# Kernel optimization log

Hardware: AMD Instinct MI355X
Metric: run time of the kernel (lower is better)

Reference implementation:

```python
import jax, jax.numpy as jnp
import numpy as np
import math

B, T, C, H = 8, 1024, 1024, 16
D = C // H  # head dim = 64
EPS = 1e-5


def layernorm(x, g, b):
    mu = jnp.mean(x, axis=-1, keepdims=True)
    var = jnp.var(x, axis=-1, keepdims=True)
    return (x - mu) * jax.lax.rsqrt(var + EPS) * g + b


def setup_inputs() -> dict:
    key = jax.random.key(0)
    ks = jax.random.split(key, 8)
    s = lambda fan_in: 1.0 / math.sqrt(fan_in)
    return {
        "x": jax.random.normal(ks[0], (B, T, C), jnp.float32),
        "Wqkv": jax.random.normal(ks[1], (C, 3 * C), jnp.float32) * s(C),
        "bqkv": jnp.zeros((3 * C,), jnp.float32),
        "Wproj": jax.random.normal(ks[2], (C, C), jnp.float32) * s(C),
        "bproj": jnp.zeros((C,), jnp.float32),
        "ln1_g": jnp.ones((C,), jnp.float32),
        "ln1_b": jnp.zeros((C,), jnp.float32),
        "ln2_g": jnp.ones((C,), jnp.float32),
        "ln2_b": jnp.zeros((C,), jnp.float32),
        "W1": jax.random.normal(ks[3], (C, 4 * C), jnp.float32) * s(C),
        "b1": jnp.zeros((4 * C,), jnp.float32),
        "W2": jax.random.normal(ks[4], (4 * C, C), jnp.float32) * s(4 * C),
        "b2": jnp.zeros((C,), jnp.float32),
    }


def reference(x, Wqkv, bqkv, Wproj, bproj, ln1_g, ln1_b, ln2_g, ln2_b, W1, b1, W2, b2):
    # --- self-attention on ln1(x) ---
    h = layernorm(x, ln1_g, ln1_b)
    qkv = h @ Wqkv + bqkv                          # [B,T,3C]
    q, k, v = jnp.split(qkv, 3, axis=-1)
    # [B,T,C] -> [B,H,T,D]
    q = q.reshape(B, T, H, D).transpose(0, 2, 1, 3)
    k = k.reshape(B, T, H, D).transpose(0, 2, 1, 3)
    v = v.reshape(B, T, H, D).transpose(0, 2, 1, 3)
    # NOTE: original uses 1/sqrt(3*n_embd//n_head), not 1/sqrt(head_dim)
    scale = 1.0 / math.sqrt(3 * C // H)
    attn = jnp.einsum("bhqd,bhkd->bhqk", q, k) * scale  # [B,H,T,T]
    causal = jnp.tril(jnp.ones((T, T), bool))
    attn = jnp.where(causal, attn, -jnp.inf)
    attn = jax.nn.softmax(attn, axis=-1)
    y = jnp.einsum("bhqk,bhkd->bhqd", attn, v)          # [B,H,T,D]
    y = y.transpose(0, 2, 1, 3).reshape(B, T, C)
    x = x + (y @ Wproj + bproj)
    # --- MLP on ln2(x) ---
    h2 = layernorm(x, ln2_g, ln2_b)
    x = x + (jax.nn.relu(h2 @ W1 + b1) @ W2 + b2)
    return x
```

## Files before the change

kernel.cpp:

```cpp
#include <hip/hip_runtime.h>

typedef __bf16 bf16;
typedef __bf16 bf16x8 __attribute__((ext_vector_type(8)));
typedef float f32x4 __attribute__((ext_vector_type(4)));

#define MFMA16(a, b, c) __builtin_amdgcn_mfma_f32_16x16x32_bf16(a, b, c, 0, 0, 0)

static constexpr int Bn = 8;
static constexpr int Tn = 1024;
static constexpr int Cn = 1024;
static constexpr int Hn = 16;

typedef const __attribute__((address_space(1))) unsigned int* gp_t;
typedef __attribute__((address_space(3))) unsigned int* lp_t;
__device__ __forceinline__ void gload_lds16(const bf16* g, bf16* l) {
    __builtin_amdgcn_global_load_lds((gp_t)(const void*)g, (lp_t)(void*)l, 16, 0, 0);
}

__global__ __launch_bounds__(256) void tcast(const float* __restrict__ in,
                                             bf16* __restrict__ out,
                                             int K, int N) {
    __shared__ float tile[32][33];
    const int n0 = blockIdx.x * 32, k0 = blockIdx.y * 32;
    const int tx = threadIdx.x & 31, ty = threadIdx.x >> 5;
#pragma unroll
    for (int i = 0; i < 4; i++)
        tile[ty + 8 * i][tx] = in[(size_t)(k0 + ty + 8 * i) * N + n0 + tx];
    __syncthreads();
#pragma unroll
    for (int i = 0; i < 4; i++)
        out[(size_t)(n0 + ty + 8 * i) * K + k0 + tx] = (bf16)tile[tx][ty + 8 * i];
}

__global__ __launch_bounds__(256) void ln_bf16(const float* __restrict__ x,
                                               const float* __restrict__ g,
                                               const float* __restrict__ be,
                                               bf16* __restrict__ out) {
    const int row = blockIdx.x, t = threadIdx.x;
    const float* xr = x + (size_t)row * Cn;
    float v[4], s = 0.f, s2 = 0.f;
#pragma unroll
    for (int i = 0; i < 4; i++) {
        v[i] = xr[t + i * 256];
        s += v[i];
        s2 += v[i] * v[i];
    }
#pragma unroll
    for (int off = 32; off > 0; off >>= 1) {
        s += __shfl_down(s, off);
        s2 += __shfl_down(s2, off);
    }
    __shared__ float red[8];
    const int wave = t >> 6, lane = t & 63;
    if (lane == 0) {
        red[wave] = s;
        red[4 + wave] = s2;
    }
    __syncthreads();
    s = red[0] + red[1] + red[2] + red[3];
    s2 = red[4] + red[5] + red[6] + red[7];
    const float mu = s * (1.f / Cn);
    const float rstd = rsqrtf(s2 * (1.f / Cn) - mu * mu + 1e-5f);
    bf16* orow = out + (size_t)row * Cn;
#pragma unroll
    for (int i = 0; i < 4; i++) {
        int c = t + i * 256;
        orow[c] = (bf16)((v[i] - mu) * rstd * g[c] + be[c]);
    }
}

__global__ __launch_bounds__(256) void vtrans(const bf16* __restrict__ qkv,
                                              bf16* __restrict__ Vt) {
    __shared__ bf16 tile[64 * 72];
    const int tid = threadIdx.x;
    const int bh = blockIdx.x, b = bh >> 4, h = bh & 15;
    const int t0 = blockIdx.y * 64;
    const int r = tid >> 3, c = (tid & 7) * 8;
#pragma unroll
    for (int i = 0; i < 2; i++) {
        const int rr = r + i * 32;
        *(bf16x8*)(tile + rr * 72 + c) =
            *(const bf16x8*)(qkv + ((size_t)(b * Tn + t0 + rr)) * 3072 + 2 * Cn + h * 64 + c);
    }
    __syncthreads();
#pragma unroll
    for (int i = 0; i < 2; i++) {
        const int d = r + i * 32;
        bf16x8 v;
#pragma unroll
        for (int j = 0; j < 8; j++) v[j] = tile[(c + j) * 72 + d];
        *(bf16x8*)(Vt + ((size_t)bh * 64 + d) * Tn + t0 + c) = v;
    }
}

template <bool RELU, bool RESID, bool OUTBF16>
__global__ __launch_bounds__(256) void gemm_bt(const bf16* __restrict__ A,
                                               const bf16* __restrict__ Bt,
                                               const float* __restrict__ bias,
                                               const float* __restrict__ resid,
                                               void* __restrict__ outp,
                                               int M, int N, int K) {
    __shared__ __align__(16) bf16 As[128 * 32];
    __shared__ __align__(16) bf16 Bs[128 * 32];
    const int t = threadIdx.x;
    const int lane = t & 63, wave = t >> 6;
    const int lane15 = lane & 15, quad = lane >> 4;
    const int m0 = blockIdx.x * 128, n0 = blockIdx.y * 128;
    const int mb = (wave >> 1) * 64, nb = (wave & 1) * 64;

    const f32x4 zero4 = {0.f, 0.f, 0.f, 0.f};
    f32x4 acc[4][4];
#pragma unroll
    for (int i = 0; i < 4; i++)
#pragma unroll
        for (int j = 0; j < 4; j++) acc[i][j] = zero4;

    const int r16 = lane >> 2, c8 = (lane & 3) * 8;
    const bf16* gA0 = A + (size_t)(m0 + wave * 16 + r16) * K + c8;
    const bf16* gA1 = gA0 + (size_t)64 * K;
    const bf16* gB0 = Bt + (size_t)(n0 + wave * 16 + r16) * K + c8;
    const bf16* gB1 = gB0 + (size_t)64 * K;
    bf16* lA0 = As + wave * 512;
    bf16* lA1 = As + 2048 + wave * 512;
    bf16* lB0 = Bs + wave * 512;
    bf16* lB1 = Bs + 2048 + wave * 512;

    for (int kt = 0; kt < K; kt += 32) {
        gload_lds16(gA0 + kt, lA0);
        gload_lds16(gA1 + kt, lA1);
        gload_lds16(gB0 + kt, lB0);
        gload_lds16(gB1 + kt, lB1);
        __syncthreads();
        bf16x8 fa[4], fb[4];
#pragma unroll
        for (int mi = 0; mi < 4; mi++)
            fa[mi] = *(const bf16x8*)(As + (mb + mi * 16 + lane15) * 32 + quad * 8);
#pragma unroll
        for (int ni = 0; ni < 4; ni++)
            fb[ni] = *(const bf16x8*)(Bs + (nb + ni * 16 + lane15) * 32 + quad * 8);
#pragma unroll
        for (int mi = 0; mi < 4; mi++)
#pragma unroll
            for (int ni = 0; ni < 4; ni++)
                acc[mi][ni] = MFMA16(fa[mi], fb[ni], acc[mi][ni]);
        __syncthreads();
    }

    float bsv[4];
#pragma unroll
    for (int ni = 0; ni < 4; ni++) bsv[ni] = bias[n0 + nb + ni * 16 + lane15];
#pragma unroll
    for (int mi = 0; mi < 4; mi++) {
#pragma unroll
        for (int reg = 0; reg < 4; reg++) {
            const int row = m0 + mb + mi * 16 + quad * 4 + reg;
#pragma unroll
            for (int ni = 0; ni < 4; ni++) {
                const int col = n0 + nb + ni * 16 + lane15;
                float v = acc[mi][ni][reg] + bsv[ni];
                if (RELU) v = v > 0.f ? v : 0.f;
                if (RESID) v += resid[(size_t)row * N + col];
                if (OUTBF16)
                    ((bf16*)outp)[(size_t)row * N + col] = (bf16)v;
                else
                    ((float*)outp)[(size_t)row * N + col] = v;
            }
        }
    }
}

__global__ __launch_bounds__(256) void attn(const bf16* __restrict__ qkv,
                                            const bf16* __restrict__ Vt,
                                            bf16* __restrict__ y) {
    __shared__ __align__(16) bf16 Ks[64 * 72];
    __shared__ __align__(16) bf16 Vs[80 * 72];
    __shared__ __align__(16) bf16 Ps[4][32 * 72];
    const int tid = threadIdx.x, lane = tid & 63, wave = tid >> 6;
    const int lane15 = lane & 15, quad = lane >> 4;
    const int b = blockIdx.x >> 4, h = blockIdx.x & 15;
    const int q0 = blockIdx.y * 128;
    const int qr0 = q0 + wave * 32;
    const float c1 = 0.10412043f;

    for (int i = tid; i < 16 * 72; i += 256)
        Vs[64 * 72 + i] = (bf16)((i < 72) ? 1.0f : 0.0f);

    bf16x8 fq[2][2];
#pragma unroll
    for (int mi = 0; mi < 2; mi++) {
        const size_t qb = ((size_t)(b * Tn + qr0 + mi * 16 + lane15)) * 3072 + h * 64;
#pragma unroll
        for (int kk = 0; kk < 2; kk++)
            fq[mi][kk] = *(const bf16x8*)(qkv + qb + kk * 32 + quad * 8);
    }

    const f32x4 zero4 = {0.f, 0.f, 0.f, 0.f};
    f32x4 o[2][4], lacc[2];
#pragma unroll
    for (int mi = 0; mi < 2; mi++) {
        lacc[mi] = zero4;
#pragma unroll
        for (int ni = 0; ni < 4; ni++) o[mi][ni] = zero4;
    }

    const int sr = tid >> 3, sc = (tid & 7) * 8;
    const int nkb = q0 / 64 + 2;
    for (int kb = 0; kb < nkb; kb++) {
        const int k0 = kb * 64;
#pragma unroll
        for (int i = 0; i < 2; i++) {
            const int r = sr + i * 32;
            *(bf16x8*)(Ks + r * 72 + sc) =
                *(const bf16x8*)(qkv + ((size_t)(b * Tn + k0 + r)) * 3072 + Cn + h * 64 + sc);
            *(bf16x8*)(Vs + r * 72 + sc) =
                *(const bf16x8*)(Vt + ((size_t)blockIdx.x * 64 + r) * Tn + k0 + sc);
        }
        __syncthreads();

        if (k0 <= qr0 + 31) {
            bf16x8 fk[4][2];
#pragma unroll
            for (int ni = 0; ni < 4; ni++)
#pragma unroll
                for (int kk = 0; kk < 2; kk++)
                    fk[ni][kk] = *(const bf16x8*)(Ks + (ni * 16 + lane15) * 72 + kk * 32 + quad * 8);
            f32x4 s[2][4];
#pragma unroll
            for (int mi = 0; mi < 2; mi++)
#pragma unroll
                for (int ni = 0; ni < 4; ni++) {
                    f32x4 a = zero4;
                    a = MFMA16(fq[mi][0], fk[ni][0], a);
                    a = MFMA16(fq[mi][1], fk[ni][1], a);
                    s[mi][ni] = a;
                }
            const bool domask = (k0 + 63 > qr0);
            if (domask) {
#pragma unroll
                for (int mi = 0; mi < 2; mi++)
#pragma unroll
                    for (int ni = 0; ni < 4; ni++)
#pragma unroll
                        for (int r = 0; r < 4; r++) {
                            const int key = k0 + ni * 16 + lane15;
                            const int row = qr0 + mi * 16 + quad * 4 + r;
                            float L = (key > row) ? -1e30f : s[mi][ni][r] * c1;
                            Ps[wave][(mi * 16 + quad * 4 + r) * 72 + ni * 16 + lane15] =
                                (bf16)__builtin_amdgcn_exp2f(L);
                        }
            } else {
#pragma unroll
                for (int mi = 0; mi < 2; mi++)
#pragma unroll
                    for (int ni = 0; ni < 4; ni++)
#pragma unroll
                        for (int r = 0; r < 4; r++)
                            Ps[wave][(mi * 16 + quad * 4 + r) * 72 + ni * 16 + lane15] =
                                (bf16)__builtin_amdgcn_exp2f(s[mi][ni][r] * c1);
            }
            bf16x8 fp[2][2];
#pragma unroll
            for (int mi = 0; mi < 2; mi++)
#pragma unroll
                for (int kk = 0; kk < 2; kk++)
                    fp[mi][kk] = *(const bf16x8*)(&Ps[wave][(mi * 16 + lane15) * 72 + kk * 32 + quad * 8]);
#pragma unroll
            for (int ni = 0; ni < 5; ni++) {
                bf16x8 fv0 = *(const bf16x8*)(Vs + (ni * 16 + lane15) * 72 + quad * 8);
                bf16x8 fv1 = *(const bf16x8*)(Vs + (ni * 16 + lane15) * 72 + 32 + quad * 8);
#pragma unroll
                for (int mi = 0; mi < 2; mi++) {
                    f32x4* dst = (ni < 4) ? &o[mi][ni] : &lacc[mi];
                    f32x4 a = *dst;
                    a = MFMA16(fp[mi][0], fv0, a);
                    a = MFMA16(fp[mi][1], fv1, a);
                    *dst = a;
                }
            }
        }
        __syncthreads();
    }

#pragma unroll
    for (int mi = 0; mi < 2; mi++)
#pragma unroll
        for (int r = 0; r < 4; r++) {
            float l = __shfl(lacc[mi][r], lane & 48);
            const float inv = 1.f / l;
            const size_t base = ((size_t)(b * Tn + qr0 + mi * 16 + quad * 4 + r)) * Cn + h * 64;
#pragma unroll
            for (int ni = 0; ni < 4; ni++)
                y[base + ni * 16 + lane15] = (bf16)(o[mi][ni][r] * inv);
        }
}

extern "C" void kernel_launch(void* const* d_in, const int* in_sizes, int n_in,
                              void* d_out, int out_size, void* d_ws, size_t ws_size,
                              hipStream_t stream) {
    const float* x = (const float*)d_in[0];
    const float* Wqkv = (const float*)d_in[1];
    const float* bqkv = (const float*)d_in[2];
    const float* Wproj = (const float*)d_in[3];
    const float* bproj = (const float*)d_in[4];
    const float* ln1g = (const float*)d_in[5];
    const float* ln1b = (const float*)d_in[6];
    const float* ln2g = (const float*)d_in[7];
    const float* ln2b = (const float*)d_in[8];
    const float* W1 = (const float*)d_in[9];
    const float* b1 = (const float*)d_in[10];
    const float* W2 = (const float*)d_in[11];
    const float* b2 = (const float*)d_in[12];
    float* out = (float*)d_out;

    char* ws = (char*)d_ws;
    size_t off = 0;
    auto alloc = [&](size_t bytes) {
        void* p = ws + off;
        off += (bytes + 255) & ~(size_t)255;
        return p;
    };
    bf16* WqkvT = (bf16*)alloc((size_t)3072 * 1024 * 2);
    bf16* WprojT = (bf16*)alloc((size_t)1024 * 1024 * 2);
    bf16* W1T = (bf16*)alloc((size_t)4096 * 1024 * 2);
    bf16* W2T = (bf16*)alloc((size_t)1024 * 4096 * 2);
    bf16* hbuf = (bf16*)alloc((size_t)8192 * 1024 * 2);
    bf16* qkvb = (bf16*)alloc((size_t)8192 * 3072 * 2);
    bf16* ybuf = (bf16*)alloc((size_t)8192 * 1024 * 2);
    bf16* vtb = (bf16*)alloc((size_t)8192 * 1024 * 2);
    float* x1 = (float*)alloc((size_t)8192 * 1024 * 4);
    bf16* a1 = qkvb;

    tcast<<<dim3(3072 / 32, 1024 / 32), 256, 0, stream>>>(Wqkv, WqkvT, 1024, 3072);
    tcast<<<dim3(1024 / 32, 1024 / 32), 256, 0, stream>>>(Wproj, WprojT, 1024, 1024);
    tcast<<<dim3(4096 / 32, 1024 / 32), 256, 0, stream>>>(W1, W1T, 1024, 4096);
    tcast<<<dim3(1024 / 32, 4096 / 32), 256, 0, stream>>>(W2, W2T, 4096, 1024);

    ln_bf16<<<8192, 256, 0, stream>>>(x, ln1g, ln1b, hbuf);
    gemm_bt<false, false, true><<<dim3(64, 24), 256, 0, stream>>>(
        hbuf, WqkvT, bqkv, nullptr, qkvb, 8192, 3072, 1024);
    vtrans<<<dim3(Bn * Hn, Tn / 64), 256, 0, stream>>>(qkvb, vtb);
    attn<<<dim3(Bn * Hn, Tn / 128), 256, 0, stream>>>(qkvb, vtb, ybuf);
    gemm_bt<false, true, false><<<dim3(64, 8), 256, 0, stream>>>(
        ybuf, WprojT, bproj, x, x1, 8192, 1024, 1024);
    ln_bf16<<<8192, 256, 0, stream>>>(x1, ln2g, ln2b, hbuf);
    gemm_bt<true, false, true><<<dim3(64, 32), 256, 0, stream>>>(
        hbuf, W1T, b1, nullptr, a1, 8192, 4096, 1024);
    gemm_bt<false, true, false><<<dim3(64, 8), 256, 0, stream>>>(
        a1, W2T, b2, x1, out, 8192, 1024, 4096);
}
```

Measured before the change: 502.7 us.

## Deepen GEMM K-tile with swizzled LDS, skip masked attention MFMAs, store x1 in bf16

The GEMM now stages 64-wide K tiles with an XOR swizzle to avoid LDS bank conflicts, and is templated on M tile height so the N=1024 GEMMs use 64-row tiles and launch more blocks. Attention skips QK and PV MFMAs for fully masked 16-wide sub-tiles on the diagonal block and writes zeros directly for them. The intermediate residual x1 is stored as bf16 instead of fp32, which halves its traffic in the LN2 and final-residual reads. The price is lower precision on the residual stream, plus more LDS per block, which may reduce occupancy.

```diff
diff --git a/kernel.cpp b/kernel.cpp
--- a/kernel.cpp
+++ b/kernel.cpp
@@ -32,16 +32,17 @@
         out[(size_t)(n0 + ty + 8 * i) * K + k0 + tx] = (bf16)tile[tx][ty + 8 * i];
 }
 
-__global__ __launch_bounds__(256) void ln_bf16(const float* __restrict__ x,
-                                               const float* __restrict__ g,
-                                               const float* __restrict__ be,
-                                               bf16* __restrict__ out) {
+template <typename T>
+__global__ __launch_bounds__(256) void ln_row(const T* __restrict__ x,
+                                              const float* __restrict__ g,
+                                              const float* __restrict__ be,
+                                              bf16* __restrict__ out) {
     const int row = blockIdx.x, t = threadIdx.x;
-    const float* xr = x + (size_t)row * Cn;
+    const T* xr = x + (size_t)row * Cn;
     float v[4], s = 0.f, s2 = 0.f;
 #pragma unroll
     for (int i = 0; i < 4; i++) {
-        v[i] = xr[t + i * 256];
+        v[i] = (float)xr[t + i * 256];
         s += v[i];
         s2 += v[i] * v[i];
     }
@@ -93,56 +94,64 @@
     }
 }
 
-template <bool RELU, bool RESID, bool OUTBF16>
+template <int TM, bool RELU, bool RESID, bool OUTBF16, typename RT>
 __global__ __launch_bounds__(256) void gemm_bt(const bf16* __restrict__ A,
                                                const bf16* __restrict__ Bt,
                                                const float* __restrict__ bias,
-                                               const float* __restrict__ resid,
+                                               const RT* __restrict__ resid,
                                                void* __restrict__ outp,
                                                int M, int N, int K) {
-    __shared__ __align__(16) bf16 As[128 * 32];
-    __shared__ __align__(16) bf16 Bs[128 * 32];
+    constexpr int MI = TM / 32;
+    constexpr int AJ = TM / 32;
+    __shared__ __align__(16) bf16 As[TM * 64];
+    __shared__ __align__(16) bf16 Bs[128 * 64];
     const int t = threadIdx.x;
     const int lane = t & 63, wave = t >> 6;
     const int lane15 = lane & 15, quad = lane >> 4;
-    const int m0 = blockIdx.x * 128, n0 = blockIdx.y * 128;
-    const int mb = (wave >> 1) * 64, nb = (wave & 1) * 64;
+    const int m0 = blockIdx.x * TM, n0 = blockIdx.y * 128;
+    const int mb = (wave >> 1) * (TM / 2), nb = (wave & 1) * 64;
 
     const f32x4 zero4 = {0.f, 0.f, 0.f, 0.f};
-    f32x4 acc[4][4];
-#pragma unroll
-    for (int i = 0; i < 4; i++)
+    f32x4 acc[MI][4];
+#pragma unroll
+    for (int i = 0; i < MI; i++)
 #pragma unroll
         for (int j = 0; j < 4; j++) acc[i][j] = zero4;
 
-    const int r16 = lane >> 2, c8 = (lane & 3) * 8;
-    const bf16* gA0 = A + (size_t)(m0 + wave * 16 + r16) * K + c8;
-    const bf16* gA1 = gA0 + (size_t)64 * K;
-    const bf16* gB0 = Bt + (size_t)(n0 + wave * 16 + r16) * K + c8;
-    const bf16* gB1 = gB0 + (size_t)64 * K;
-    bf16* lA0 = As + wave * 512;
-    bf16* lA1 = As + 2048 + wave * 512;
-    bf16* lB0 = Bs + wave * 512;
-    bf16* lB1 = Bs + 2048 + wave * 512;
-
-    for (int kt = 0; kt < K; kt += 32) {
-        gload_lds16(gA0 + kt, lA0);
-        gload_lds16(gA1 + kt, lA1);
-        gload_lds16(gB0 + kt, lB0);
-        gload_lds16(gB1 + kt, lB1);
+    const int grow = lane >> 3;
+    const int gcol = ((lane & 7) ^ grow) * 8;
+    const bf16* gA = A + (size_t)(m0 + wave * (AJ * 8) + grow) * K + gcol;
+    const bf16* gB = Bt + (size_t)(n0 + wave * 32 + grow) * K + gcol;
+    bf16* lA = As + (wave * AJ) * 512;
+    bf16* lB = Bs + (wave * 4) * 512;
+
+    for (int kt = 0; kt < K; kt += 64) {
+#pragma unroll
+        for (int j = 0; j < AJ; j++)
+            gload_lds16(gA + (size_t)(j * 8) * K + kt, lA + j * 512);
+#pragma unroll
+        for (int j = 0; j < 4; j++)
+            gload_lds16(gB + (size_t)(j * 8) * K + kt, lB + j * 512);
         __syncthreads();
-        bf16x8 fa[4], fb[4];
-#pragma unroll
-        for (int mi = 0; mi < 4; mi++)
-            fa[mi] = *(const bf16x8*)(As + (mb + mi * 16 + lane15) * 32 + quad * 8);
-#pragma unroll
-        for (int ni = 0; ni < 4; ni++)
-            fb[ni] = *(const bf16x8*)(Bs + (nb + ni * 16 + lane15) * 32 + quad * 8);
-#pragma unroll
-        for (int mi = 0; mi < 4; mi++)
-#pragma unroll
-            for (int ni = 0; ni < 4; ni++)
-                acc[mi][ni] = MFMA16(fa[mi], fb[ni], acc[mi][ni]);
+#pragma unroll
+        for (int kk = 0; kk < 2; kk++) {
+            bf16x8 fa[MI], fb[4];
+#pragma unroll
+            for (int mi = 0; mi < MI; mi++) {
+                const int r = mb + mi * 16 + lane15;
+                fa[mi] = *(const bf16x8*)(As + r * 64 + (((kk * 4 + quad) ^ (r & 7)) * 8));
+            }
+#pragma unroll
+            for (int ni = 0; ni < 4; ni++) {
+                const int r = nb + ni * 16 + lane15;
+                fb[ni] = *(const bf16x8*)(Bs + r * 64 + (((kk * 4 + quad) ^ (r & 7)) * 8));
+            }
+#pragma unroll
+            for (int mi = 0; mi < MI; mi++)
+#pragma unroll
+                for (int ni = 0; ni < 4; ni++)
+                    acc[mi][ni] = MFMA16(fa[mi], fb[ni], acc[mi][ni]);
+        }
         __syncthreads();
     }
 
@@ -150,7 +159,7 @@
 #pragma unroll
     for (int ni = 0; ni < 4; ni++) bsv[ni] = bias[n0 + nb + ni * 16 + lane15];
 #pragma unroll
-    for (int mi = 0; mi < 4; mi++) {
+    for (int mi = 0; mi < MI; mi++) {
 #pragma unroll
         for (int reg = 0; reg < 4; reg++) {
             const int row = m0 + mb + mi * 16 + quad * 4 + reg;
@@ -159,7 +168,7 @@
                 const int col = n0 + nb + ni * 16 + lane15;
                 float v = acc[mi][ni][reg] + bsv[ni];
                 if (RELU) v = v > 0.f ? v : 0.f;
-                if (RESID) v += resid[(size_t)row * N + col];
+                if (RESID) v += (float)resid[(size_t)row * N + col];
                 if (OUTBF16)
                     ((bf16*)outp)[(size_t)row * N + col] = (bf16)v;
                 else
@@ -229,25 +238,37 @@
             for (int mi = 0; mi < 2; mi++)
 #pragma unroll
                 for (int ni = 0; ni < 4; ni++) {
-                    f32x4 a = zero4;
-                    a = MFMA16(fq[mi][0], fk[ni][0], a);
-                    a = MFMA16(fq[mi][1], fk[ni][1], a);
-                    s[mi][ni] = a;
+                    if (k0 + ni * 16 <= qr0 + mi * 16 + 15) {
+                        f32x4 a = zero4;
+                        a = MFMA16(fq[mi][0], fk[ni][0], a);
+                        a = MFMA16(fq[mi][1], fk[ni][1], a);
+                        s[mi][ni] = a;
+                    }
                 }
             const bool domask = (k0 + 63 > qr0);
             if (domask) {
 #pragma unroll
                 for (int mi = 0; mi < 2; mi++)
 #pragma unroll
-                    for (int ni = 0; ni < 4; ni++)
-#pragma unroll
-                        for (int r = 0; r < 4; r++) {
+                    for (int ni = 0; ni < 4; ni++) {
+                        bf16* pd = &Ps[wave][(mi * 16 + quad * 4) * 72 + ni * 16 + lane15];
+                        if (k0 + ni * 16 > qr0 + mi * 16 + 15) {
+#pragma unroll
+                            for (int r = 0; r < 4; r++) pd[r * 72] = (bf16)0.f;
+                        } else if (k0 + ni * 16 + 15 <= qr0 + mi * 16) {
+#pragma unroll
+                            for (int r = 0; r < 4; r++)
+                                pd[r * 72] = (bf16)__builtin_amdgcn_exp2f(s[mi][ni][r] * c1);
+                        } else {
                             const int key = k0 + ni * 16 + lane15;
-                            const int row = qr0 + mi * 16 + quad * 4 + r;
-                            float L = (key > row) ? -1e30f : s[mi][ni][r] * c1;
-                            Ps[wave][(mi * 16 + quad * 4 + r) * 72 + ni * 16 + lane15] =
-                                (bf16)__builtin_amdgcn_exp2f(L);
+                            const int row0 = qr0 + mi * 16 + quad * 4;
+#pragma unroll
+                            for (int r = 0; r < 4; r++) {
+                                float L = (key > row0 + r) ? -1e30f : s[mi][ni][r] * c1;
+                                pd[r * 72] = (bf16)__builtin_amdgcn_exp2f(L);
+                            }
                         }
+                    }
             } else {
 #pragma unroll
                 for (int mi = 0; mi < 2; mi++)
@@ -264,6 +285,7 @@
 #pragma unroll
                 for (int kk = 0; kk < 2; kk++)
                     fp[mi][kk] = *(const bf16x8*)(&Ps[wave][(mi * 16 + lane15) * 72 + kk * 32 + quad * 8]);
+            const bool use_kk1 = (k0 + 32 <= qr0 + 31);
 #pragma unroll
             for (int ni = 0; ni < 5; ni++) {
                 bf16x8 fv0 = *(const bf16x8*)(Vs + (ni * 16 + lane15) * 72 + quad * 8);
@@ -273,7 +295,7 @@
                     f32x4* dst = (ni < 4) ? &o[mi][ni] : &lacc[mi];
                     f32x4 a = *dst;
                     a = MFMA16(fp[mi][0], fv0, a);
-                    a = MFMA16(fp[mi][1], fv1, a);
+                    if (use_kk1) a = MFMA16(fp[mi][1], fv1, a);
                     *dst = a;
                 }
             }
@@ -327,7 +349,7 @@
     bf16* qkvb = (bf16*)alloc((size_t)8192 * 3072 * 2);
     bf16* ybuf = (bf16*)alloc((size_t)8192 * 1024 * 2);
     bf16* vtb = (bf16*)alloc((size_t)8192 * 1024 * 2);
-    float* x1 = (float*)alloc((size_t)8192 * 1024 * 4);
+    bf16* x1b = (bf16*)alloc((size_t)8192 * 1024 * 2);
     bf16* a1 = qkvb;
 
     tcast<<<dim3(3072 / 32, 1024 / 32), 256, 0, stream>>>(Wqkv, WqkvT, 1024, 3072);
@@ -335,16 +357,16 @@
     tcast<<<dim3(4096 / 32, 1024 / 32), 256, 0, stream>>>(W1, W1T, 1024, 4096);
     tcast<<<dim3(1024 / 32, 4096 / 32), 256, 0, stream>>>(W2, W2T, 4096, 1024);
 
-    ln_bf16<<<8192, 256, 0, stream>>>(x, ln1g, ln1b, hbuf);
-    gemm_bt<false, false, true><<<dim3(64, 24), 256, 0, stream>>>(
-        hbuf, WqkvT, bqkv, nullptr, qkvb, 8192, 3072, 1024);
+    ln_row<float><<<8192, 256, 0, stream>>>(x, ln1g, ln1b, hbuf);
+    gemm_bt<128, false, false, true, float><<<dim3(64, 24), 256, 0, stream>>>(
+        hbuf, WqkvT, bqkv, (const float*)nullptr, qkvb, 8192, 3072, 1024);
     vtrans<<<dim3(Bn * Hn, Tn / 64), 256, 0, stream>>>(qkvb, vtb);
     attn<<<dim3(Bn * Hn, Tn / 128), 256, 0, stream>>>(qkvb, vtb, ybuf);
-    gemm_bt<false, true, false><<<dim3(64, 8), 256, 0, stream>>>(
-        ybuf, WprojT, bproj, x, x1, 8192, 1024, 1024);
-    ln_bf16<<<8192, 256, 0, stream>>>(x1, ln2g, ln2b, hbuf);
-    gemm_bt<true, false, true><<<dim3(64, 32), 256, 0, stream>>>(
-        hbuf, W1T, b1, nullptr, a1, 8192, 4096, 1024);
-    gemm_bt<false, true, false><<<dim3(64, 8), 256, 0, stream>>>(
-        a1, W2T, b2, x1, out, 8192, 1024, 4096);
-}
+    gemm_bt<64, false, true, true, float><<<dim3(128, 8), 256, 0, stream>>>(
+        ybuf, WprojT, bproj, x, x1b, 8192, 1024, 1024);
+    ln_row<bf16><<<8192, 256, 0, stream>>>(x1b, ln2g, ln2b, hbuf);
+    gemm_bt<128, true, false, true, float><<<dim3(64, 32), 256, 0, stream>>>(
+        hbuf, W1T, b1, (const float*)nullptr, a1, 8192, 4096, 1024);
+    gemm_bt<64, false, true, false, bf16><<<dim3(128, 8), 256, 0, stream>>>(
+        a1, W2T, b2, x1b, out, 8192, 1024, 4096);
+}
```

Result: faster. 469.1 us (-6.7%).
